# Kernel optimization log

Measured on AMD Instinct MI355X. Metric: run time of the kernel, lower is better.

The kernel has to match this reference:

```python
import jax, jax.numpy as jnp
import numpy as np

H = W = 128
R = 2
H2, W2 = H // R, W // R
TOPK = 3
NSEG = H * W + 1  # segment 0 = background


def _ccl(binary):
    """8-connected component labeling via iterative max-label propagation.
    binary: [H,W] bool. Returns int32 labels, 0 = background; each component
    gets a unique (arbitrary) positive id = max pixel index in the component."""
    idx = jnp.arange(1, H * W + 1, dtype=jnp.int32).reshape(H, W)
    lab0 = jnp.where(binary, idx, 0)

    def cond(c):
        return c[1]

    def body(c):
        lab, _ = c
        nb = jax.lax.reduce_window(lab, jnp.int32(0), jax.lax.max,
                                   (3, 3), (1, 1), 'SAME')  # 3x3 incl. self
        new = jnp.where(binary, nb, 0)
        return new, jnp.any(new != lab)

    lab, _ = jax.lax.while_loop(cond, body, (lab0, jnp.bool_(True)))
    return lab


def _process_one(prob_i, feat_i):
    """prob_i: [1,H,W], feat_i: [Cf,H,W] -> [3*Cf, H2, W2]."""
    p = prob_i[0]
    binary = p > 0.5
    lab = _ccl(binary).reshape(-1)  # [H*W] segment ids

    ones = jnp.ones((H * W,), jnp.float32)
    count = jax.ops.segment_sum(ones, lab, num_segments=NSEG)
    conf_sum = jax.ops.segment_sum(p.reshape(-1), lab, num_segments=NSEG)
    mean_conf = conf_sum / jnp.maximum(count, 1.0)

    rows = jnp.repeat(jnp.arange(H, dtype=jnp.int32), W)
    cols = jnp.tile(jnp.arange(W, dtype=jnp.int32), H)
    min_r = jax.ops.segment_min(rows, lab, num_segments=NSEG)
    max_r = jax.ops.segment_max(rows, lab, num_segments=NSEG)
    min_c = jax.ops.segment_min(cols, lab, num_segments=NSEG)
    max_c = jax.ops.segment_max(cols, lab, num_segments=NSEG)

    valid = (count > 0) & (jnp.arange(NSEG) > 0)
    score = jnp.where(valid, mean_conf, -jnp.inf)
    _, top_idx = jax.lax.top_k(score, TOPK)  # regions sorted by mean confidence
    K = jnp.sum(valid.astype(jnp.int32))     # number of connected regions

    # duplication rules: K==0 -> full image x3; K==1 -> [f0,f0,f0];
    # K==2 -> [f0,f0,f1]; K>=3 -> [f0,f1,f2]
    i0, i1 = top_idx[0], top_idx[1]
    slots = jnp.where(K >= 3, top_idx,
            jnp.where(K == 2, jnp.stack([i0, i0, i1]),
                      jnp.stack([i0, i0, i0])))

    mr = jnp.where(K > 0, min_r[slots], 0)
    Mr = jnp.where(K > 0, max_r[slots] + 1, H)  # bbox half-open, regionprops style
    mc = jnp.where(K > 0, min_c[slots], 0)
    Mc = jnp.where(K > 0, max_c[slots] + 1, W)

    def crop(a, b, c, d):
        # PyTorch nearest interpolate: src = floor(dst * in/out)
        r = a + (jnp.arange(H2) * (b - a)) // H2
        cc = c + (jnp.arange(W2) * (d - c)) // W2
        return feat_i[:, r][:, :, cc]  # [Cf, H2, W2]

    out = jax.vmap(crop)(mr, Mr, mc, Mc)  # [3, Cf, H2, W2]
    return out.reshape(-1, H2, W2)         # [3*Cf, H2, W2]


def setup_inputs() -> dict:
    key = jax.random.key(0)
    k1, k2 = jax.random.split(key)
    prob = jax.random.uniform(k1, (16, 1, H, W), dtype=jnp.float32)
    feat = jax.random.normal(k2, (16, 192, H, W), dtype=jnp.float32)
    return {"prob": prob, "feat": feat}


def reference(prob, feat):
    return jax.vmap(_process_one)(prob, feat)  # [B, 3*Cf, H2, W2]
```

## Files before the change

### kernel.cpp

```cpp
#include <hip/hip_runtime.h>
#include <limits.h>

#define HH 128
#define WW_ 128
#define HW 16384
#define NB 16
#define CF 192
#define H2 64
#define W2 64
#define NRUN 8192
#define NCOMP 4096

typedef float vf4 __attribute__((ext_vector_type(4)));
typedef unsigned long long ull;


__device__ inline int uf_find(int* par, int x) {
    volatile int* vp = (volatile int*)par;
    int p = vp[x];
    while (p != x) {
        int g = vp[p];
        vp[x] = g;
        x = g;
        p = vp[x];
    }
    return x;
}

__device__ inline void uf_union(int* par, int a, int b) {
    int ra = uf_find(par, a);
    int rb = uf_find(par, b);
    while (ra != rb) {
        if (ra < rb) { int t = ra; ra = rb; rb = t; }
        int old = atomicCAS(&par[ra], ra, rb);
        if (old == ra) return;
        ra = uf_find(par, old);
        rb = uf_find(par, rb);
    }
}

__device__ inline int walk_term(int* par, int x) {
    volatile int* vp = (volatile int*)par;
    int p = vp[x];
    while (p < NRUN && p != x) { x = p; p = vp[x]; }
    return (p >= NRUN) ? p : x;
}


__device__ inline int getbit2(ull lo, ull hi, int c) {
    return (int)(((c < 64) ? (lo >> c) : (hi >> (c - 64))) & 1ULL);
}

__device__ inline int leading_ones(ull v) {
    ull nv = ~v;
    return (nv == 0ULL) ? 64 : __clzll(nv);
}

__device__ inline int trailing_ones(ull v) {
    ull nv = ~v;
    return (nv == 0ULL) ? 64 : (__ffsll(nv) - 1);
}

__device__ inline int run_start_col(ull lo, ull hi, int c) {
    if (c < 64) {
        int ones = leading_ones(lo << (63 - c));
        return c - ones + 1;
    }
    int ones = leading_ones(hi << (127 - c));
    int rs = c - ones + 1;
    if (rs == 64) rs -= leading_ones(lo);
    return rs;
}

__device__ inline int run_end_col(ull lo, ull hi, int c) {
    if (c >= 64) {
        return c + trailing_ones(hi >> (c - 64)) - 1;
    }
    int e = c + trailing_ones(lo >> c) - 1;
    if (e == 63) e += trailing_ones(hi);
    return e;
}

__device__ inline int run_index(ull rs_lo, ull rs_hi, int cs) {
    if (cs < 64)  return __popcll(rs_lo & ((1ULL << cs) - 1ULL));
    if (cs == 64) return __popcll(rs_lo);
    return __popcll(rs_lo) + __popcll(rs_hi & ((1ULL << (cs - 64)) - 1ULL));
}

__device__ inline void span_mask(int a, int b, ull& mlo, ull& mhi) {
    ull one = ~0ULL;
    int bl = (b < 63) ? b : 63;
    mlo = (a <= 63) ? (((bl == 63) ? one : ((1ULL << (bl + 1)) - 1)) & ~((1ULL << a) - 1)) : 0ULL;
    if (b >= 64) {
        int a2 = (a >= 64) ? a - 64 : 0;
        int b2 = b - 64;
        mhi = ((b2 == 63) ? one : ((1ULL << (b2 + 1)) - 1)) & ~((1ULL << a2) - 1);
    } else mhi = 0ULL;
}

__device__ inline void top3_ins(float s, int id, int x,
    float& s0, float& s1, float& s2,
    int& i0, int& i1, int& i2,
    int& x0, int& x1, int& x2)
{
    if (x < 0) return;
    if (s > s0 || (s == s0 && id < i0)) {
        s2 = s1; i2 = i1; x2 = x1;
        s1 = s0; i1 = i0; x1 = x0;
        s0 = s;  i0 = id; x0 = x;
    } else if (s > s1 || (s == s1 && id < i1)) {
        s2 = s1; i2 = i1; x2 = x1;
        s1 = s;  i1 = id; x1 = x;
    } else if (s > s2 || (s == s2 && id < i2)) {
        s2 = s;  i2 = id; x2 = x;
    }
}


__global__ __launch_bounds__(1024) void ccl_kernel(
    const float* __restrict__ prob, int* __restrict__ bbox)
{
    __shared__ int parent[NRUN];
    __shared__ ull rowmask[HH][2];
    __shared__ ull rsmask[HH][2];
    __shared__ int nrunrow[HH];
    __shared__ int   lcnt[NCOMP];
    __shared__ float lconf[NCOMP];
    __shared__ int lminr[NCOMP], lmaxr[NCOMP];
    __shared__ int lminc[NCOMP], lmaxc[NCOMP];
    __shared__ int lmaxid[NCOMP];
    __shared__ int snroots;
    __shared__ float wss[48];
    __shared__ int wid_[48], wrx[48];

    const int b = blockIdx.x;
    const int tid = threadIdx.x;
    const int lane = tid & 63;
    const float* p = prob + (size_t)b * HW;

    if (tid == 0) snroots = 0;

    {
        int wv = tid >> 6;
        #pragma unroll
        for (int k = 0; k < 8; ++k) {
            int row = wv * 8 + k;
            const float* rp = p + (row << 7);
            ull m0 = __ballot(rp[lane] > 0.5f);
            ull m1 = __ballot(rp[64 + lane] > 0.5f);
            if (lane == 0) {
                rowmask[row][0] = m0; rowmask[row][1] = m1;
                ull rs_lo = m0 & ~(m0 << 1);
                ull rs_hi = m1 & ~((m1 << 1) | (m0 >> 63));
                rsmask[row][0] = rs_lo; rsmask[row][1] = rs_hi;
                nrunrow[row] = __popcll(rs_lo) + __popcll(rs_hi);
            }
        }
        #pragma unroll
        for (int k = 0; k < NRUN / 1024; ++k)
            parent[k * 1024 + tid] = k * 1024 + tid;
    }
    __syncthreads();

    {
        int row = tid >> 3;
        int w0 = (tid & 7) * 16;
        if (row > 0) {
            ull lo = rowmask[row][0], hi = rowmask[row][1];
            ull rs_lo = rsmask[row][0], rs_hi = rsmask[row][1];
            ull seg = ((w0 < 64) ? (rs_lo >> w0) : (rs_hi >> (w0 - 64))) & 0xFFFFULL;
            if (seg) {
                ull ulo = rowmask[row - 1][0], uhi = rowmask[row - 1][1];
                ull urs_lo = rsmask[row - 1][0], urs_hi = rsmask[row - 1][1];
                int ub = (row - 1) << 6;
                while (seg) {
                    int c = w0 + (__ffsll(seg) - 1);
                    seg &= seg - 1;
                    int e = run_end_col(lo, hi, c);
                    int rid = (row << 6) + run_index(rs_lo, rs_hi, c);
                    int s0 = (c > 0) ? c - 1 : 0;
                    int s1 = (e < 127) ? e + 1 : 127;
                    if (getbit2(ulo, uhi, s0))
                        uf_union(parent, rid,
                                 ub + run_index(urs_lo, urs_hi, run_start_col(ulo, uhi, s0)));
                    if (s1 > s0) {
                        ull mlo, mhi;
                        span_mask(s0 + 1, s1, mlo, mhi);
                        ull h_lo = urs_lo & mlo, h_hi = urs_hi & mhi;
                        while (h_lo) {
                            int cs = __ffsll(h_lo) - 1; h_lo &= h_lo - 1;
                            uf_union(parent, rid, ub + run_index(urs_lo, urs_hi, cs));
                        }
                        while (h_hi) {
                            int cs = 64 + __ffsll(h_hi) - 1; h_hi &= h_hi - 1;
                            uf_union(parent, rid, ub + run_index(urs_lo, urs_hi, cs));
                        }
                    }
                }
            }
        }
    }
    __syncthreads();

    for (int rid = tid; rid < NRUN; rid += 1024) {
        bool valid = (rid & 63) < nrunrow[rid >> 6];
        bool isroot = valid && parent[rid] == rid;
        ull m = __ballot(isroot);
        if (m) {
            int baseIdx = 0;
            if (lane == 0) baseIdx = atomicAdd(&snroots, __popcll(m));
            baseIdx = __shfl(baseIdx, 0);
            if (isroot)
                parent[rid] = NRUN + baseIdx + __popcll(m & ((1ULL << lane) - 1ULL));
        }
        if (valid && !isroot)
            parent[rid] = walk_term(parent, rid);
    }
    __syncthreads();

    const int n = snroots;
    for (int j = tid; j < n; j += 1024) {
        lcnt[j] = 0; lconf[j] = 0.f;
        lminr[j] = INT_MAX; lmaxr[j] = -1;
        lminc[j] = INT_MAX; lmaxc[j] = -1;
        lmaxid[j] = 0;
    }
    __syncthreads();

    {
        int row = tid >> 3;
        int w0 = (tid & 7) * 16;
        ull lo = rowmask[row][0], hi = rowmask[row][1];
        ull rs_lo = rsmask[row][0], rs_hi = rsmask[row][1];
        ull seg = ((w0 < 64) ? (rs_lo >> w0) : (rs_hi >> (w0 - 64))) & 0xFFFFULL;
        while (seg) {
            int c = w0 + (__ffsll(seg) - 1);
            seg &= seg - 1;
            int e = run_end_col(lo, hi, c);
            int rid = (row << 6) + run_index(rs_lo, rs_hi, c);
            int v = parent[rid];
            int idx = (v >= NRUN) ? (v - NRUN) : (parent[v] - NRUN);
            float s = 0.f;
            for (int j = c; j <= e; ++j) s += p[(row << 7) + j];
            atomicAdd(&lcnt[idx], e - c + 1);
            atomicAdd(&lconf[idx], s);
            atomicMin(&lminr[idx], row);
            atomicMax(&lmaxr[idx], row);
            atomicMin(&lminc[idx], c);
            atomicMax(&lmaxc[idx], e);
            atomicMax(&lmaxid[idx], (row << 7) + e + 1);
        }
    }
    __syncthreads();

    {
        float s0 = -INFINITY, s1 = -INFINITY, s2 = -INFINITY;
        int i0 = INT_MAX, i1 = INT_MAX, i2 = INT_MAX;
        int x0 = -1, x1 = -1, x2 = -1;
        for (int j = tid; j < n; j += 1024) {
            float s = lconf[j] / (float)lcnt[j];
            top3_ins(s, lmaxid[j], j, s0, s1, s2, i0, i1, i2, x0, x1, x2);
        }
        for (int off = 32; off; off >>= 1) {
            float bs0 = __shfl_xor(s0, off), bs1 = __shfl_xor(s1, off), bs2 = __shfl_xor(s2, off);
            int bi0 = __shfl_xor(i0, off), bi1 = __shfl_xor(i1, off), bi2 = __shfl_xor(i2, off);
            int bx0 = __shfl_xor(x0, off), bx1 = __shfl_xor(x1, off), bx2 = __shfl_xor(x2, off);
            top3_ins(bs0, bi0, bx0, s0, s1, s2, i0, i1, i2, x0, x1, x2);
            top3_ins(bs1, bi1, bx1, s0, s1, s2, i0, i1, i2, x0, x1, x2);
            top3_ins(bs2, bi2, bx2, s0, s1, s2, i0, i1, i2, x0, x1, x2);
        }
        if (lane == 0) {
            int w = tid >> 6;
            wss[w * 3 + 0] = s0; wid_[w * 3 + 0] = i0; wrx[w * 3 + 0] = x0;
            wss[w * 3 + 1] = s1; wid_[w * 3 + 1] = i1; wrx[w * 3 + 1] = x1;
            wss[w * 3 + 2] = s2; wid_[w * 3 + 2] = i2; wrx[w * 3 + 2] = x2;
        }
    }
    __syncthreads();

    if (tid == 0) {
        float t0 = -INFINITY, t1 = -INFINITY, t2 = -INFINITY;
        int ti0 = INT_MAX, ti1 = INT_MAX, ti2 = INT_MAX;
        int tx0 = -1, tx1 = -1, tx2 = -1;
        for (int t = 0; t < 48; ++t)
            top3_ins(wss[t], wid_[t], wrx[t], t0, t1, t2, ti0, ti1, ti2, tx0, tx1, tx2);
        int K = n;
        int roots[3];
        if (K >= 3)      { roots[0] = tx0; roots[1] = tx1; roots[2] = tx2; }
        else if (K == 2) { roots[0] = tx0; roots[1] = tx0; roots[2] = tx1; }
        else             { roots[0] = tx0; roots[1] = tx0; roots[2] = tx0; }
        for (int slot = 0; slot < 3; ++slot) {
            int mr, h, mc, w;
            if (K == 0) { mr = 0; h = HH; mc = 0; w = WW_; }
            else {
                int rt = roots[slot];
                mr = lminr[rt]; h = lmaxr[rt] + 1 - mr;
                mc = lminc[rt]; w = lmaxc[rt] + 1 - mc;
            }
            int* o = bbox + (b * 3 + slot) * 4;
            o[0] = mr; o[1] = h; o[2] = mc; o[3] = w;
        }
    }
}


__global__ __launch_bounds__(256) void crop_kernel(
    const float* __restrict__ feat, const int* __restrict__ bbox,
    float* __restrict__ out)
{
    const int gid = blockIdx.x * 256 + threadIdx.x;
    const int o4 = gid * 2;
    const int x4 = o4 & 15;
    const int y  = (o4 >> 4) & 63;
    const int t  = o4 >> 10;
    const int c  = t % CF;
    const int bs = t / CF;
    const int* bb = bbox + bs * 4;
    const int mr = bb[0], h = bb[1], mc = bb[2], w = bb[3];
    const int r = mr + ((y * h) >> 6);
    const int bimg = bs / 3;
    const float* row = feat + (((size_t)bimg * CF + c) * HH + r) * WW_;
    const int x = x4 * 4;
    vf4 v0, v1;
    v0.x = row[mc + (((x + 0) * w) >> 6)];
    v0.y = row[mc + (((x + 1) * w) >> 6)];
    v0.z = row[mc + (((x + 2) * w) >> 6)];
    v0.w = row[mc + (((x + 3) * w) >> 6)];
    v1.x = row[mc + (((x + 4) * w) >> 6)];
    v1.y = row[mc + (((x + 5) * w) >> 6)];
    v1.z = row[mc + (((x + 6) * w) >> 6)];
    v1.w = row[mc + (((x + 7) * w) >> 6)];
    __builtin_nontemporal_store(v0, (vf4*)out + o4);
    __builtin_nontemporal_store(v1, (vf4*)out + o4 + 1);
}


extern "C" void kernel_launch(void* const* d_in, const int* in_sizes, int n_in,
                              void* d_out, int out_size, void* d_ws, size_t ws_size,
                              hipStream_t stream) {
    const float* prob = (const float*)d_in[0];
    const float* feat = (const float*)d_in[1];
    float* out = (float*)d_out;

    int* bbox = (int*)d_ws;

    hipLaunchKernelGGL(ccl_kernel, dim3(NB), dim3(1024), 0, stream,
                       prob, bbox);
    const int total4 = NB * 3 * CF * H2 * (W2 / 4);
    hipLaunchKernelGGL(crop_kernel, dim3(total4 / 512), dim3(256), 0, stream,
                       feat, bbox, out);
}
```

Measured before the change: 392.6 us.

## Split per-image CCL into parallel strip labeling plus boundary merge kernel

```diff
diff --git a/kernel.cpp b/kernel.cpp
--- a/kernel.cpp
+++ b/kernel.cpp
@@ -8,8 +8,10 @@
 #define CF 192
 #define H2 64
 #define W2 64
-#define NRUN 8192
-#define NCOMP 4096
+#define SH 16
+#define NS 8
+#define SRUN 1024
+#define GSPACE 8192
 
 typedef float vf4 __attribute__((ext_vector_type(4)));
 typedef unsigned long long ull;
@@ -39,11 +41,11 @@
     }
 }
 
-__device__ inline int walk_term(int* par, int x) {
+__device__ inline int walk_term(int* par, int x, int thr) {
     volatile int* vp = (volatile int*)par;
     int p = vp[x];
-    while (p < NRUN && p != x) { x = p; p = vp[x]; }
-    return (p >= NRUN) ? p : x;
+    while (p < thr && p != x) { x = p; p = vp[x]; }
+    return (p >= thr) ? p : x;
 }
 
 
@@ -117,54 +119,52 @@
 }
 
 
-__global__ __launch_bounds__(1024) void ccl_kernel(
-    const float* __restrict__ prob, int* __restrict__ bbox)
+__global__ __launch_bounds__(256) void strip_kernel(
+    const float* __restrict__ prob,
+    int* __restrict__ ncomp,
+    int* __restrict__ rec_cnt, float* __restrict__ rec_conf,
+    int* __restrict__ rec_minr, int* __restrict__ rec_maxr,
+    int* __restrict__ rec_minc, int* __restrict__ rec_maxc,
+    int* __restrict__ rec_maxid,
+    int* __restrict__ topmap, int* __restrict__ botmap,
+    ull* __restrict__ bmasks)
 {
-    __shared__ int parent[NRUN];
-    __shared__ ull rowmask[HH][2];
-    __shared__ ull rsmask[HH][2];
-    __shared__ int nrunrow[HH];
-    __shared__ int   lcnt[NCOMP];
-    __shared__ float lconf[NCOMP];
-    __shared__ int lminr[NCOMP], lmaxr[NCOMP];
-    __shared__ int lminc[NCOMP], lmaxc[NCOMP];
-    __shared__ int lmaxid[NCOMP];
-    __shared__ int snroots;
-    __shared__ float wss[48];
-    __shared__ int wid_[48], wrx[48];
-
-    const int b = blockIdx.x;
-    const int tid = threadIdx.x;
-    const int lane = tid & 63;
-    const float* p = prob + (size_t)b * HW;
-
-    if (tid == 0) snroots = 0;
-
-    {
-        int wv = tid >> 6;
-        #pragma unroll
-        for (int k = 0; k < 8; ++k) {
-            int row = wv * 8 + k;
-            const float* rp = p + (row << 7);
-            ull m0 = __ballot(rp[lane] > 0.5f);
-            ull m1 = __ballot(rp[64 + lane] > 0.5f);
-            if (lane == 0) {
-                rowmask[row][0] = m0; rowmask[row][1] = m1;
-                ull rs_lo = m0 & ~(m0 << 1);
-                ull rs_hi = m1 & ~((m1 << 1) | (m0 >> 63));
-                rsmask[row][0] = rs_lo; rsmask[row][1] = rs_hi;
-                nrunrow[row] = __popcll(rs_lo) + __popcll(rs_hi);
-            }
-        }
-        #pragma unroll
-        for (int k = 0; k < NRUN / 1024; ++k)
-            parent[k * 1024 + tid] = k * 1024 + tid;
-    }
-    __syncthreads();
-
-    {
-        int row = tid >> 3;
-        int w0 = (tid & 7) * 16;
+    __shared__ ull rowmask[SH][2], rsmask[SH][2];
+    __shared__ int nrunrow[SH];
+    __shared__ int parent[SRUN];
+    __shared__ int   lcnt[SRUN];
+    __shared__ float lconf[SRUN];
+    __shared__ int lminr[SRUN], lmaxr[SRUN], lminc[SRUN], lmaxc[SRUN], lmaxid[SRUN];
+    __shared__ int sn;
+
+    const int sg = blockIdx.x;
+    const int b = sg >> 3, s = sg & 7;
+    const int row0 = s * SH;
+    const int tid = threadIdx.x, lane = tid & 63, wv = tid >> 6;
+    const float* p = prob + (size_t)b * HW + (size_t)row0 * WW_;
+
+    if (tid == 0) sn = 0;
+
+    #pragma unroll
+    for (int k = 0; k < 4; ++k) {
+        int row = wv * 4 + k;
+        ull m0 = __ballot(p[(row << 7) + lane] > 0.5f);
+        ull m1 = __ballot(p[(row << 7) + 64 + lane] > 0.5f);
+        if (lane == 0) {
+            rowmask[row][0] = m0; rowmask[row][1] = m1;
+            ull rs_lo = m0 & ~(m0 << 1);
+            ull rs_hi = m1 & ~((m1 << 1) | (m0 >> 63));
+            rsmask[row][0] = rs_lo; rsmask[row][1] = rs_hi;
+            nrunrow[row] = __popcll(rs_lo) + __popcll(rs_hi);
+        }
+    }
+    #pragma unroll
+    for (int k = 0; k < SRUN / 256; ++k)
+        parent[k * 256 + tid] = k * 256 + tid;
+    __syncthreads();
+
+    if (tid < 128) {
+        int row = tid >> 3, w0 = (tid & 7) * 16;
         if (row > 0) {
             ull lo = rowmask[row][0], hi = rowmask[row][1];
             ull rs_lo = rsmask[row][0], rs_hi = rsmask[row][1];
@@ -178,14 +178,14 @@
                     seg &= seg - 1;
                     int e = run_end_col(lo, hi, c);
                     int rid = (row << 6) + run_index(rs_lo, rs_hi, c);
-                    int s0 = (c > 0) ? c - 1 : 0;
-                    int s1 = (e < 127) ? e + 1 : 127;
-                    if (getbit2(ulo, uhi, s0))
+                    int a0 = (c > 0) ? c - 1 : 0;
+                    int a1 = (e < 127) ? e + 1 : 127;
+                    if (getbit2(ulo, uhi, a0))
                         uf_union(parent, rid,
-                                 ub + run_index(urs_lo, urs_hi, run_start_col(ulo, uhi, s0)));
-                    if (s1 > s0) {
+                                 ub + run_index(urs_lo, urs_hi, run_start_col(ulo, uhi, a0)));
+                    if (a1 > a0) {
                         ull mlo, mhi;
-                        span_mask(s0 + 1, s1, mlo, mhi);
+                        span_mask(a0 + 1, a1, mlo, mhi);
                         ull h_lo = urs_lo & mlo, h_hi = urs_hi & mhi;
                         while (h_lo) {
                             int cs = __ffsll(h_lo) - 1; h_lo &= h_lo - 1;
@@ -202,24 +202,24 @@
     }
     __syncthreads();
 
-    for (int rid = tid; rid < NRUN; rid += 1024) {
+    for (int rid = tid; rid < SRUN; rid += 256) {
         bool valid = (rid & 63) < nrunrow[rid >> 6];
         bool isroot = valid && parent[rid] == rid;
         ull m = __ballot(isroot);
         if (m) {
             int baseIdx = 0;
-            if (lane == 0) baseIdx = atomicAdd(&snroots, __popcll(m));
+            if (lane == 0) baseIdx = atomicAdd(&sn, __popcll(m));
             baseIdx = __shfl(baseIdx, 0);
             if (isroot)
-                parent[rid] = NRUN + baseIdx + __popcll(m & ((1ULL << lane) - 1ULL));
+                parent[rid] = SRUN + baseIdx + __popcll(m & ((1ULL << lane) - 1ULL));
         }
         if (valid && !isroot)
-            parent[rid] = walk_term(parent, rid);
-    }
-    __syncthreads();
-
-    const int n = snroots;
-    for (int j = tid; j < n; j += 1024) {
+            parent[rid] = walk_term(parent, rid, SRUN);
+    }
+    __syncthreads();
+
+    const int n = sn;
+    for (int j = tid; j < n; j += 256) {
         lcnt[j] = 0; lconf[j] = 0.f;
         lminr[j] = INT_MAX; lmaxr[j] = -1;
         lminc[j] = INT_MAX; lmaxc[j] = -1;
@@ -227,9 +227,9 @@
     }
     __syncthreads();
 
-    {
-        int row = tid >> 3;
-        int w0 = (tid & 7) * 16;
+    if (tid < 128) {
+        int row = tid >> 3, w0 = (tid & 7) * 16;
+        int gr = row0 + row;
         ull lo = rowmask[row][0], hi = rowmask[row][1];
         ull rs_lo = rsmask[row][0], rs_hi = rsmask[row][1];
         ull seg = ((w0 < 64) ? (rs_lo >> w0) : (rs_hi >> (w0 - 64))) & 0xFFFFULL;
@@ -239,16 +239,152 @@
             int e = run_end_col(lo, hi, c);
             int rid = (row << 6) + run_index(rs_lo, rs_hi, c);
             int v = parent[rid];
-            int idx = (v >= NRUN) ? (v - NRUN) : (parent[v] - NRUN);
-            float s = 0.f;
-            for (int j = c; j <= e; ++j) s += p[(row << 7) + j];
+            int idx = (v >= SRUN) ? (v - SRUN) : (parent[v] - SRUN);
+            float sum = 0.f;
+            for (int j = c; j <= e; ++j) sum += p[(row << 7) + j];
             atomicAdd(&lcnt[idx], e - c + 1);
-            atomicAdd(&lconf[idx], s);
-            atomicMin(&lminr[idx], row);
-            atomicMax(&lmaxr[idx], row);
+            atomicAdd(&lconf[idx], sum);
+            atomicMin(&lminr[idx], gr);
+            atomicMax(&lmaxr[idx], gr);
             atomicMin(&lminc[idx], c);
             atomicMax(&lmaxc[idx], e);
-            atomicMax(&lmaxid[idx], (row << 7) + e + 1);
+            atomicMax(&lmaxid[idx], (gr << 7) + e + 1);
+        }
+    }
+    __syncthreads();
+
+    const size_t rb = (size_t)sg * SRUN;
+    for (int d = tid; d < n; d += 256) {
+        rec_cnt[rb + d]   = lcnt[d];
+        rec_conf[rb + d]  = lconf[d];
+        rec_minr[rb + d]  = lminr[d];
+        rec_maxr[rb + d]  = lmaxr[d];
+        rec_minc[rb + d]  = lminc[d];
+        rec_maxc[rb + d]  = lmaxc[d];
+        rec_maxid[rb + d] = lmaxid[d];
+    }
+    if (tid == 0) ncomp[sg] = n;
+    if (tid < 64) {
+        if (tid < nrunrow[0]) {
+            int v = parent[tid];
+            topmap[sg * 64 + tid] = (v >= SRUN) ? (v - SRUN) : (parent[v] - SRUN);
+        }
+        if (tid < nrunrow[SH - 1]) {
+            int rid = ((SH - 1) << 6) + tid;
+            int v = parent[rid];
+            botmap[sg * 64 + tid] = (v >= SRUN) ? (v - SRUN) : (parent[v] - SRUN);
+        }
+    }
+    if (tid >= 64 && tid < 72) {
+        int k = tid - 64;
+        ull v = 0;
+        switch (k) {
+            case 0: v = rowmask[0][0]; break;
+            case 1: v = rowmask[0][1]; break;
+            case 2: v = rsmask[0][0];  break;
+            case 3: v = rsmask[0][1];  break;
+            case 4: v = rowmask[SH-1][0]; break;
+            case 5: v = rowmask[SH-1][1]; break;
+            case 6: v = rsmask[SH-1][0];  break;
+            case 7: v = rsmask[SH-1][1];  break;
+        }
+        bmasks[sg * 8 + k] = v;
+    }
+}
+
+
+__global__ __launch_bounds__(1024) void merge_kernel(
+    const int* __restrict__ ncomp,
+    const int* __restrict__ rec_cnt, const float* __restrict__ rec_conf,
+    const int* __restrict__ rec_minr, const int* __restrict__ rec_maxr,
+    const int* __restrict__ rec_minc, const int* __restrict__ rec_maxc,
+    const int* __restrict__ rec_maxid,
+    const int* __restrict__ topmap, const int* __restrict__ botmap,
+    const ull* __restrict__ bmasks,
+    int* __restrict__ bbox)
+{
+    __shared__ int parent[GSPACE];
+    __shared__ int   lcnt[GSPACE];
+    __shared__ float lconf[GSPACE];
+    __shared__ int lmaxid[GSPACE];
+    __shared__ int nc[NS];
+    __shared__ float wss[48];
+    __shared__ int wid_[48], wrx[48];
+    __shared__ int winner[3], w_minr[3], w_maxr[3], w_minc[3], w_maxc[3];
+    __shared__ int sK;
+
+    const int b = blockIdx.x;
+    const int tid = threadIdx.x, lane = tid & 63;
+
+    if (tid == 0) sK = 0;
+    if (tid < NS) nc[tid] = ncomp[b * 8 + tid];
+    __syncthreads();
+
+    for (int g = tid; g < GSPACE; g += 1024) {
+        parent[g] = g;
+        int s = g >> 10, d = g & 1023;
+        if (d < nc[s]) {
+            size_t rb = (size_t)(b * 8 + s) * SRUN + d;
+            lcnt[g] = rec_cnt[rb];
+            lconf[g] = rec_conf[rb];
+            lmaxid[g] = rec_maxid[rb];
+        }
+    }
+    __syncthreads();
+
+    if (tid < 56) {
+        int i = tid >> 3, w0 = (tid & 7) * 16;
+        int sgb = b * 8 + i;
+        int sgt = b * 8 + i + 1;
+        ull tm_lo = bmasks[sgt*8+0], tm_hi = bmasks[sgt*8+1];
+        ull trs_lo = bmasks[sgt*8+2], trs_hi = bmasks[sgt*8+3];
+        ull bm_lo = bmasks[sgb*8+4], bm_hi = bmasks[sgb*8+5];
+        ull brs_lo = bmasks[sgb*8+6], brs_hi = bmasks[sgb*8+7];
+        ull seg = ((w0 < 64) ? (trs_lo >> w0) : (trs_hi >> (w0 - 64))) & 0xFFFFULL;
+        while (seg) {
+            int c = w0 + (__ffsll(seg) - 1);
+            seg &= seg - 1;
+            int e = run_end_col(tm_lo, tm_hi, c);
+            int g_top = ((i + 1) << 10) + topmap[sgt * 64 + run_index(trs_lo, trs_hi, c)];
+            int a0 = (c > 0) ? c - 1 : 0;
+            int a1 = (e < 127) ? e + 1 : 127;
+            if (getbit2(bm_lo, bm_hi, a0)) {
+                int g_bot = (i << 10) +
+                    botmap[sgb * 64 + run_index(brs_lo, brs_hi, run_start_col(bm_lo, bm_hi, a0))];
+                uf_union(parent, g_top, g_bot);
+            }
+            if (a1 > a0) {
+                ull mlo, mhi;
+                span_mask(a0 + 1, a1, mlo, mhi);
+                ull h_lo = brs_lo & mlo, h_hi = brs_hi & mhi;
+                while (h_lo) {
+                    int cs = __ffsll(h_lo) - 1; h_lo &= h_lo - 1;
+                    uf_union(parent, g_top, (i << 10) + botmap[sgb * 64 + run_index(brs_lo, brs_hi, cs)]);
+                }
+                while (h_hi) {
+                    int cs = 64 + __ffsll(h_hi) - 1; h_hi &= h_hi - 1;
+                    uf_union(parent, g_top, (i << 10) + botmap[sgb * 64 + run_index(brs_lo, brs_hi, cs)]);
+                }
+            }
+        }
+    }
+    __syncthreads();
+
+    for (int g = tid; g < GSPACE; g += 1024) {
+        int s = g >> 10, d = g & 1023;
+        if (d < nc[s]) parent[g] = uf_find(parent, g);
+    }
+    __syncthreads();
+
+    for (int g = tid; g < GSPACE; g += 1024) {
+        int s = g >> 10, d = g & 1023;
+        if (d < nc[s]) {
+            int rg = parent[g];
+            if (rg != g) {
+                atomicAdd(&lcnt[rg], lcnt[g]);
+                atomicAdd(&lconf[rg], lconf[g]);
+                atomicMax(&lmaxid[rg], lmaxid[g]);
+            }
         }
     }
     __syncthreads();
@@ -257,14 +393,20 @@
         float s0 = -INFINITY, s1 = -INFINITY, s2 = -INFINITY;
         int i0 = INT_MAX, i1 = INT_MAX, i2 = INT_MAX;
         int x0 = -1, x1 = -1, x2 = -1;
-        for (int j = tid; j < n; j += 1024) {
-            float s = lconf[j] / (float)lcnt[j];
-            top3_ins(s, lmaxid[j], j, s0, s1, s2, i0, i1, i2, x0, x1, x2);
+        int myK = 0;
+        for (int g = tid; g < GSPACE; g += 1024) {
+            int s = g >> 10, d = g & 1023;
+            if (d < nc[s] && parent[g] == g) {
+                myK++;
+                float sc = lconf[g] / (float)lcnt[g];
+                top3_ins(sc, lmaxid[g], g, s0, s1, s2, i0, i1, i2, x0, x1, x2);
+            }
         }
         for (int off = 32; off; off >>= 1) {
             float bs0 = __shfl_xor(s0, off), bs1 = __shfl_xor(s1, off), bs2 = __shfl_xor(s2, off);
             int bi0 = __shfl_xor(i0, off), bi1 = __shfl_xor(i1, off), bi2 = __shfl_xor(i2, off);
             int bx0 = __shfl_xor(x0, off), bx1 = __shfl_xor(x1, off), bx2 = __shfl_xor(x2, off);
+            myK += __shfl_xor(myK, off);
             top3_ins(bs0, bi0, bx0, s0, s1, s2, i0, i1, i2, x0, x1, x2);
             top3_ins(bs1, bi1, bx1, s0, s1, s2, i0, i1, i2, x0, x1, x2);
             top3_ins(bs2, bi2, bx2, s0, s1, s2, i0, i1, i2, x0, x1, x2);
@@ -274,6 +416,7 @@
             wss[w * 3 + 0] = s0; wid_[w * 3 + 0] = i0; wrx[w * 3 + 0] = x0;
             wss[w * 3 + 1] = s1; wid_[w * 3 + 1] = i1; wrx[w * 3 + 1] = x1;
             wss[w * 3 + 2] = s2; wid_[w * 3 + 2] = i2; wrx[w * 3 + 2] = x2;
+            atomicAdd(&sK, myK);
         }
     }
     __syncthreads();
@@ -284,22 +427,53 @@
         int tx0 = -1, tx1 = -1, tx2 = -1;
         for (int t = 0; t < 48; ++t)
             top3_ins(wss[t], wid_[t], wrx[t], t0, t1, t2, ti0, ti1, ti2, tx0, tx1, tx2);
-        int K = n;
-        int roots[3];
-        if (K >= 3)      { roots[0] = tx0; roots[1] = tx1; roots[2] = tx2; }
-        else if (K == 2) { roots[0] = tx0; roots[1] = tx0; roots[2] = tx1; }
-        else             { roots[0] = tx0; roots[1] = tx0; roots[2] = tx0; }
-        for (int slot = 0; slot < 3; ++slot) {
-            int mr, h, mc, w;
-            if (K == 0) { mr = 0; h = HH; mc = 0; w = WW_; }
-            else {
-                int rt = roots[slot];
-                mr = lminr[rt]; h = lmaxr[rt] + 1 - mr;
-                mc = lminc[rt]; w = lmaxc[rt] + 1 - mc;
+        int K = sK;
+        if (K >= 3)      { winner[0] = tx0; winner[1] = tx1; winner[2] = tx2; }
+        else if (K == 2) { winner[0] = tx0; winner[1] = tx0; winner[2] = tx1; }
+        else if (K == 1) { winner[0] = tx0; winner[1] = tx0; winner[2] = tx0; }
+        else             { winner[0] = -1;  winner[1] = -1;  winner[2] = -1;  }
+    }
+    if (tid >= 64 && tid < 67) {
+        int s = tid - 64;
+        w_minr[s] = INT_MAX; w_maxr[s] = -1;
+        w_minc[s] = INT_MAX; w_maxc[s] = -1;
+    }
+    __syncthreads();
+
+    {
+        int wn0 = winner[0], wn1 = winner[1], wn2 = winner[2];
+        for (int g = tid; g < GSPACE; g += 1024) {
+            int s = g >> 10, d = g & 1023;
+            if (d >= nc[s]) continue;
+            int rg = parent[g];
+            if (rg != wn0 && rg != wn1 && rg != wn2) continue;
+            size_t rb = (size_t)(b * 8 + s) * SRUN + d;
+            int mnr = rec_minr[rb], mxr = rec_maxr[rb];
+            int mnc = rec_minc[rb], mxc = rec_maxc[rb];
+            #pragma unroll
+            for (int sl = 0; sl < 3; ++sl) {
+                int wn = (sl == 0) ? wn0 : (sl == 1) ? wn1 : wn2;
+                if (rg == wn) {
+                    atomicMin(&w_minr[sl], mnr);
+                    atomicMax(&w_maxr[sl], mxr);
+                    atomicMin(&w_minc[sl], mnc);
+                    atomicMax(&w_maxc[sl], mxc);
+                }
             }
-            int* o = bbox + (b * 3 + slot) * 4;
-            o[0] = mr; o[1] = h; o[2] = mc; o[3] = w;
-        }
+        }
+    }
+    __syncthreads();
+
+    if (tid < 3) {
+        int sl = tid;
+        int mr, h, mc, w;
+        if (winner[sl] < 0) { mr = 0; h = HH; mc = 0; w = WW_; }
+        else {
+            mr = w_minr[sl]; h = w_maxr[sl] + 1 - mr;
+            mc = w_minc[sl]; w = w_maxc[sl] + 1 - mc;
+        }
+        int* o = bbox + (b * 3 + sl) * 4;
+        o[0] = mr; o[1] = h; o[2] = mc; o[3] = w;
     }
 }
 
@@ -342,10 +516,29 @@
     const float* feat = (const float*)d_in[1];
     float* out = (float*)d_out;
 
-    int* bbox = (int*)d_ws;
-
-    hipLaunchKernelGGL(ccl_kernel, dim3(NB), dim3(1024), 0, stream,
-                       prob, bbox);
+    char* ws = (char*)d_ws;
+    const size_t NREC = 128 * (size_t)SRUN;
+    int*   bbox      = (int*)(ws);
+    ull*   bmasks    = (ull*)(ws + 1024);
+    int*   ncomp     = (int*)(ws + 1024 + 8192);
+    int*   topmap    = (int*)(ws + 16384);
+    int*   botmap    = (int*)(ws + 16384 + 32768);
+    char*  recbase   = ws + 16384 + 65536;
+    int*   rec_cnt   = (int*)(recbase + 0 * NREC * 4);
+    float* rec_conf  = (float*)(recbase + 1 * NREC * 4);
+    int*   rec_minr  = (int*)(recbase + 2 * NREC * 4);
+    int*   rec_maxr  = (int*)(recbase + 3 * NREC * 4);
+    int*   rec_minc  = (int*)(recbase + 4 * NREC * 4);
+    int*   rec_maxc  = (int*)(recbase + 5 * NREC * 4);
+    int*   rec_maxid = (int*)(recbase + 6 * NREC * 4);
+
+    hipLaunchKernelGGL(strip_kernel, dim3(NB * NS), dim3(256), 0, stream,
+                       prob, ncomp, rec_cnt, rec_conf, rec_minr, rec_maxr,
+                       rec_minc, rec_maxc, rec_maxid, topmap, botmap, bmasks);
+    hipLaunchKernelGGL(merge_kernel, dim3(NB), dim3(1024), 0, stream,
+                       ncomp, rec_cnt, rec_conf, rec_minr, rec_maxr,
+                       rec_minc, rec_maxc, rec_maxid, topmap, botmap, bmasks,
+                       bbox);
     const int total4 = NB * 3 * CF * H2 * (W2 / 4);
     hipLaunchKernelGGL(crop_kernel, dim3(total4 / 512), dim3(256), 0, stream,
                        feat, bbox, out);
```

Result: slower. 401.5 us (+2.3%).
